# Performance work log

Measured on AMD Instinct MI355X. Metric: run time of the kernel, lower is better.

## Reference

```python
import jax, jax.numpy as jnp
import numpy as np

IN_NF, IN_EF, OUT_NF, H1, H2, H_IN = 16, 8, 16, 8, 8, 16
N_NODES, N_EDGES = 100000, 2000000


def _mlp(x, w1, b1, w2, b2):
    # Linear -> LeakyReLU(0.2) -> Linear
    return jax.nn.leaky_relu(x @ w1 + b1, negative_slope=0.2) @ w2 + b2


def setup_inputs() -> dict:
    key = jax.random.key(0)
    ks = jax.random.split(key, 20)
    d_in = 2 * IN_NF + IN_EF  # 40
    inp = {
        "nf": jax.random.normal(ks[0], (N_NODES, IN_NF), jnp.float32),
        "src_out": jax.random.randint(ks[1], (N_EDGES,), 0, N_NODES),
        "dst_out": jax.random.randint(ks[2], (N_EDGES,), 0, N_NODES),
        "nef_out": jax.random.normal(ks[3], (N_EDGES, IN_EF), jnp.float32),
        "src_in": jax.random.randint(ks[4], (N_EDGES,), 0, N_NODES),
        "dst_in": jax.random.randint(ks[5], (N_EDGES,), 0, N_NODES),
        "nef_in": jax.random.normal(ks[6], (N_EDGES, IN_EF), jnp.float32),
        # MLP_msg_o2i: (2*in_nf+in_ef) -> h_in -> out_nf
        "w_o2i1": jax.random.normal(ks[7], (d_in, H_IN), jnp.float32) * 0.1,
        "b_o2i1": jnp.zeros((H_IN,), jnp.float32),
        "w_o2i2": jax.random.normal(ks[8], (H_IN, OUT_NF), jnp.float32) * 0.1,
        "b_o2i2": jnp.zeros((OUT_NF,), jnp.float32),
        # MLP_msg_i2o: (2*in_nf+in_ef) -> h_in -> 1+h1+h2
        "w_i2o1": jax.random.normal(ks[9], (d_in, H_IN), jnp.float32) * 0.1,
        "b_i2o1": jnp.zeros((H_IN,), jnp.float32),
        "w_i2o2": jax.random.normal(ks[10], (H_IN, 1 + H1 + H2), jnp.float32) * 0.1,
        "b_i2o2": jnp.zeros((1 + H1 + H2,), jnp.float32),
        # MLP_reduce_o: (in_nf+h1+h2) -> h_in -> out_nf  (note: in_nf==out_nf here)
        "w_red1": jax.random.normal(ks[11], (OUT_NF + H1 + H2, H_IN), jnp.float32) * 0.1,
        "b_red1": jnp.zeros((H_IN,), jnp.float32),
        "w_red2": jax.random.normal(ks[12], (H_IN, OUT_NF), jnp.float32) * 0.1,
        "b_red2": jnp.zeros((OUT_NF,), jnp.float32),
    }
    return inp


def reference(nf, src_out, dst_out, nef_out, src_in, dst_in, nef_in,
              w_o2i1, b_o2i1, w_o2i2, b_o2i2,
              w_i2o1, b_i2o1, w_i2o2, b_i2o2,
              w_red1, b_red1, w_red2, b_red2):
    n = nf.shape[0]
    # --- update_all over 'net_out': edge gather-concat -> MLP -> scatter sum
    x_o = jnp.concatenate([nf[src_out], nf[dst_out], nef_out], axis=1)  # [E, 40]
    efi = _mlp(x_o, w_o2i1, b_o2i1, w_o2i2, b_o2i2)                      # [E, out_nf]
    new_nf = jax.ops.segment_sum(efi, dst_out, num_segments=n)           # overwrites 'new_nf'
    # --- apply_edges over 'net_in': gated messages
    x_i = jnp.concatenate([nf[src_in], nf[dst_in], nef_in], axis=1)      # [E, 40]
    m = _mlp(x_i, w_i2o1, b_i2o1, w_i2o2, b_i2o2)                        # [E, 1+h1+h2]
    k = jax.nn.sigmoid(m[:, :1])
    efo1 = m[:, 1:1 + H1] * k
    efo2 = m[:, 1 + H1:] * k
    # --- scatter sum / mean into dst nodes
    nfo1 = jax.ops.segment_sum(efo1, dst_in, num_segments=n)
    cnt = jax.ops.segment_sum(jnp.ones((dst_in.shape[0],), nf.dtype), dst_in, num_segments=n)
    nfo2 = jax.ops.segment_sum(efo2, dst_in, num_segments=n) / jnp.maximum(cnt, 1.0)[:, None]
    # --- apply_nodes only on net_in destination nodes; others keep new_nf
    reduced = _mlp(jnp.concatenate([new_nf, nfo1, nfo2], axis=1), w_red1, b_red1, w_red2, b_red2)
    has_in = (cnt > 0)[:, None]
    return jnp.where(has_in, reduced, new_nf)
```

## Files before the change

kernel.cpp:

```cpp
#include <hip/hip_runtime.h>
#include <math.h>

#define IN_NF 16
#define IN_EF 8
#define OUT_NF 16
#define H1 8
#define H2 8
#define H_IN 16
#define D_IN 40
#define NT 4
#define SCAN_NB 128

__device__ __forceinline__ unsigned int f2bf_bits(float f) {
    unsigned int u = __float_as_uint(f);
    u += 0x7FFFu + ((u >> 16) & 1u);
    return u >> 16;
}
__device__ __forceinline__ float bf_lo(unsigned int w) { return __uint_as_float(w << 16); }
__device__ __forceinline__ float bf_hi(unsigned int w) { return __uint_as_float(w & 0xFFFF0000u); }

__device__ __forceinline__ void unpack16(const unsigned short* base, float* x) {
    const uint4* p = (const uint4*)base;
    uint4 a = p[0], b = p[1];
    x[0]=bf_lo(a.x);  x[1]=bf_hi(a.x);  x[2]=bf_lo(a.y);  x[3]=bf_hi(a.y);
    x[4]=bf_lo(a.z);  x[5]=bf_hi(a.z);  x[6]=bf_lo(a.w);  x[7]=bf_hi(a.w);
    x[8]=bf_lo(b.x);  x[9]=bf_hi(b.x);  x[10]=bf_lo(b.y); x[11]=bf_hi(b.y);
    x[12]=bf_lo(b.z); x[13]=bf_hi(b.z); x[14]=bf_lo(b.w); x[15]=bf_hi(b.w);
}

__global__ __launch_bounds__(256) void k_tobf16(
    const float* __restrict__ nf, unsigned short* __restrict__ nf16, int n_nodes)
{
    int n = blockIdx.x * blockDim.x + threadIdx.x;
    if (n >= n_nodes) return;
    const float4* p = (const float4*)(nf + (long)n * IN_NF);
    unsigned int w[8];
#pragma unroll
    for (int q = 0; q < 4; ++q) {
        float4 v = p[q];
        w[2*q+0] = f2bf_bits(v.x) | (f2bf_bits(v.y) << 16);
        w[2*q+1] = f2bf_bits(v.z) | (f2bf_bits(v.w) << 16);
    }
    uint4* o = (uint4*)(nf16 + (size_t)n * 16);
    o[0] = make_uint4(w[0], w[1], w[2], w[3]);
    o[1] = make_uint4(w[4], w[5], w[6], w[7]);
}

__global__ __launch_bounds__(256) void k_hist(
    const int* __restrict__ dst_out, const int* __restrict__ dst_in,
    int* __restrict__ off_out, int* __restrict__ off_in, int n_edges)
{
    int i = (blockIdx.x * blockDim.x + threadIdx.x) * 4;
    if (i + 3 < n_edges) {
        int4 a = *(const int4*)(dst_out + i);
        atomicAdd(&off_out[a.x], 1); atomicAdd(&off_out[a.y], 1);
        atomicAdd(&off_out[a.z], 1); atomicAdd(&off_out[a.w], 1);
        int4 b = *(const int4*)(dst_in + i);
        atomicAdd(&off_in[b.x], 1); atomicAdd(&off_in[b.y], 1);
        atomicAdd(&off_in[b.z], 1); atomicAdd(&off_in[b.w], 1);
    } else {
        for (int e = i; e < n_edges; ++e) {
            atomicAdd(&off_out[dst_out[e]], 1);
            atomicAdd(&off_in[dst_in[e]], 1);
        }
    }
}

__global__ __launch_bounds__(256) void k_scan_partial(
    const int* __restrict__ a0, const int* __restrict__ a1, int n,
    int* __restrict__ bsum)
{
    int arr = blockIdx.x >> 7;
    int blk = blockIdx.x & (SCAN_NB - 1);
    const int* a = arr ? a1 : a0;
    int chunk = (n + SCAN_NB - 1) / SCAN_NB;
    int beg = blk * chunk;
    int end = min(beg + chunk, n);
    int s = 0;
    for (int i = beg + threadIdx.x; i < end; i += 256) s += a[i];
    __shared__ int sm[256];
    int t = threadIdx.x;
    sm[t] = s;
    __syncthreads();
    for (int d = 128; d > 0; d >>= 1) {
        if (t < d) sm[t] += sm[t + d];
        __syncthreads();
    }
    if (t == 0) bsum[arr * SCAN_NB + blk] = sm[0];
}

__global__ __launch_bounds__(64) void k_scan_bsum(int* __restrict__ bsum)
{
    int arr = threadIdx.x;
    if (arr >= 2) return;
    int run = 0;
    for (int i = 0; i < SCAN_NB; ++i) {
        int v = bsum[arr * SCAN_NB + i];
        bsum[arr * SCAN_NB + i] = run;
        run += v;
    }
}

__global__ __launch_bounds__(256) void k_scan_final(
    int* __restrict__ a0, int* __restrict__ a1, int n,
    const int* __restrict__ bsum)
{
    int arr = blockIdx.x >> 7;
    int blk = blockIdx.x & (SCAN_NB - 1);
    int* a = arr ? a1 : a0;
    int chunk = (n + SCAN_NB - 1) / SCAN_NB;
    int beg = blk * chunk;
    int end = min(beg + chunk, n);
    int t = threadIdx.x;
    __shared__ int sm[256];
    __shared__ int carry_sm;
    if (t == 0) carry_sm = bsum[arr * SCAN_NB + blk];
    __syncthreads();
    for (int base = beg; base < end; base += 256) {
        int i = base + t;
        int v = (i < end) ? a[i] : 0;
        sm[t] = v;
        __syncthreads();
        for (int d = 1; d < 256; d <<= 1) {
            int u = (t >= d) ? sm[t - d] : 0;
            __syncthreads();
            sm[t] += u;
            __syncthreads();
        }
        int carry = carry_sm;
        if (i < end) a[i] = carry + sm[t] - v;
        __syncthreads();
        if (t == 0) carry_sm = carry + sm[255];
        __syncthreads();
    }
}

__global__ __launch_bounds__(256, 4) void k_edge_a(
    const unsigned short* __restrict__ nf16,
    const int* __restrict__ src, const int* __restrict__ dst,
    const float* __restrict__ nef,
    const float* __restrict__ W1, const float* __restrict__ B1,
    const float* __restrict__ W2, const float* __restrict__ B2,
    int* __restrict__ cursor, unsigned short* __restrict__ msg, int n_edges)
{
    int e = blockIdx.x * blockDim.x + threadIdx.x;
    if (e >= n_edges) return;
    int s = src[e];
    int d = dst[e];

    float xs[IN_NF], xd[IN_NF], xe[IN_EF];
    unpack16(nf16 + (size_t)s * 16, xs);
    unpack16(nf16 + (size_t)d * 16, xd);
    {
        const float4* pe = (const float4*)(nef + (long)e * IN_EF);
#pragma unroll
        for (int q = 0; q < 2; ++q) {
            float4 v = pe[q];
            xe[4*q+0]=v.x; xe[4*q+1]=v.y; xe[4*q+2]=v.z; xe[4*q+3]=v.w;
        }
    }

    float h[H_IN];
#pragma unroll
    for (int j = 0; j < H_IN; ++j) h[j] = B1[j];
#pragma unroll
    for (int k = 0; k < IN_NF; ++k) {
        float a0 = xs[k], a1 = xd[k];
#pragma unroll
        for (int j = 0; j < H_IN; ++j) {
            h[j] = fmaf(a0, W1[k * H_IN + j], h[j]);
            h[j] = fmaf(a1, W1[(IN_NF + k) * H_IN + j], h[j]);
        }
    }
#pragma unroll
    for (int k = 0; k < IN_EF; ++k) {
        float a0 = xe[k];
#pragma unroll
        for (int j = 0; j < H_IN; ++j)
            h[j] = fmaf(a0, W1[(2 * IN_NF + k) * H_IN + j], h[j]);
    }
#pragma unroll
    for (int j = 0; j < H_IN; ++j) h[j] = (h[j] >= 0.f) ? h[j] : 0.2f * h[j];

    float o[OUT_NF];
#pragma unroll
    for (int j = 0; j < OUT_NF; ++j) o[j] = B2[j];
#pragma unroll
    for (int k = 0; k < H_IN; ++k) {
        float hk = h[k];
#pragma unroll
        for (int j = 0; j < OUT_NF; ++j) o[j] = fmaf(hk, W2[k * OUT_NF + j], o[j]);
    }

    int p = atomicAdd(&cursor[d], 1);
    unsigned int w[8];
#pragma unroll
    for (int q = 0; q < 8; ++q)
        w[q] = f2bf_bits(o[2 * q]) | (f2bf_bits(o[2 * q + 1]) << 16);
    uint4* pm = (uint4*)(msg + (size_t)p * 16);
    pm[0] = make_uint4(w[0], w[1], w[2], w[3]);
    pm[1] = make_uint4(w[4], w[5], w[6], w[7]);
}

__global__ __launch_bounds__(256, 4) void k_edge_b(
    const unsigned short* __restrict__ nf16,
    const int* __restrict__ src, const int* __restrict__ dst,
    const float* __restrict__ nef,
    const float* __restrict__ W1, const float* __restrict__ B1,
    const float* __restrict__ W2, const float* __restrict__ B2,
    int* __restrict__ cursor, unsigned short* __restrict__ msg, int n_edges)
{
    int e = blockIdx.x * blockDim.x + threadIdx.x;
    if (e >= n_edges) return;
    int s = src[e];
    int d = dst[e];

    float xs[IN_NF], xd[IN_NF], xe[IN_EF];
    unpack16(nf16 + (size_t)s * 16, xs);
    unpack16(nf16 + (size_t)d * 16, xd);
    {
        const float4* pe = (const float4*)(nef + (long)e * IN_EF);
#pragma unroll
        for (int q = 0; q < 2; ++q) {
            float4 v = pe[q];
            xe[4*q+0]=v.x; xe[4*q+1]=v.y; xe[4*q+2]=v.z; xe[4*q+3]=v.w;
        }
    }

    float h[H_IN];
#pragma unroll
    for (int j = 0; j < H_IN; ++j) h[j] = B1[j];
#pragma unroll
    for (int k = 0; k < IN_NF; ++k) {
        float a0 = xs[k], a1 = xd[k];
#pragma unroll
        for (int j = 0; j < H_IN; ++j) {
            h[j] = fmaf(a0, W1[k * H_IN + j], h[j]);
            h[j] = fmaf(a1, W1[(IN_NF + k) * H_IN + j], h[j]);
        }
    }
#pragma unroll
    for (int k = 0; k < IN_EF; ++k) {
        float a0 = xe[k];
#pragma unroll
        for (int j = 0; j < H_IN; ++j)
            h[j] = fmaf(a0, W1[(2 * IN_NF + k) * H_IN + j], h[j]);
    }
#pragma unroll
    for (int j = 0; j < H_IN; ++j) h[j] = (h[j] >= 0.f) ? h[j] : 0.2f * h[j];

    const int M = 1 + H1 + H2;
    float o[17];
#pragma unroll
    for (int j = 0; j < M; ++j) o[j] = B2[j];
#pragma unroll
    for (int k = 0; k < H_IN; ++k) {
        float hk = h[k];
#pragma unroll
        for (int j = 0; j < M; ++j) o[j] = fmaf(hk, W2[k * M + j], o[j]);
    }
    float g = 1.f / (1.f + __expf(-o[0]));

    int p = atomicAdd(&cursor[d], 1);
    unsigned int w[8];
#pragma unroll
    for (int q = 0; q < 8; ++q)
        w[q] = f2bf_bits(o[1 + 2*q] * g) | (f2bf_bits(o[2 + 2*q] * g) << 16);
    uint4* pm = (uint4*)(msg + (size_t)p * 16);
    pm[0] = make_uint4(w[0], w[1], w[2], w[3]);
    pm[1] = make_uint4(w[4], w[5], w[6], w[7]);
}

__global__ __launch_bounds__(256, 4) void k_gather(
    const int* __restrict__ curA, const int* __restrict__ curB,
    const unsigned short* __restrict__ msgA, const unsigned short* __restrict__ msgB,
    const float* __restrict__ w_red1, const float* __restrict__ b_red1,
    const float* __restrict__ w_red2, const float* __restrict__ b_red2,
    float* __restrict__ out, int n_nodes)
{
    int tid = blockIdx.x * blockDim.x + threadIdx.x;
    int node = tid >> 2;
    int t = tid & (NT - 1);
    if (node >= n_nodes) return;

    int begA = (node == 0) ? 0 : curA[node - 1];
    int endA = curA[node];
    int begB = (node == 0) ? 0 : curB[node - 1];
    int endB = curB[node];

    float accA[16], accB[16];
#pragma unroll
    for (int j = 0; j < 16; ++j) { accA[j] = 0.f; accB[j] = 0.f; }

    for (int i = begA + t; i < endA; i += NT) {
        const uint4* p = (const uint4*)(msgA + (size_t)i * 16);
        uint4 v0 = p[0], v1 = p[1];
        unsigned int w0=v0.x,w1=v0.y,w2=v0.z,w3=v0.w,w4=v1.x,w5=v1.y,w6=v1.z,w7=v1.w;
        accA[0]+=bf_lo(w0); accA[1]+=bf_hi(w0); accA[2]+=bf_lo(w1); accA[3]+=bf_hi(w1);
        accA[4]+=bf_lo(w2); accA[5]+=bf_hi(w2); accA[6]+=bf_lo(w3); accA[7]+=bf_hi(w3);
        accA[8]+=bf_lo(w4); accA[9]+=bf_hi(w4); accA[10]+=bf_lo(w5); accA[11]+=bf_hi(w5);
        accA[12]+=bf_lo(w6); accA[13]+=bf_hi(w6); accA[14]+=bf_lo(w7); accA[15]+=bf_hi(w7);
    }
    for (int i = begB + t; i < endB; i += NT) {
        const uint4* p = (const uint4*)(msgB + (size_t)i * 16);
        uint4 v0 = p[0], v1 = p[1];
        unsigned int w0=v0.x,w1=v0.y,w2=v0.z,w3=v0.w,w4=v1.x,w5=v1.y,w6=v1.z,w7=v1.w;
        accB[0]+=bf_lo(w0); accB[1]+=bf_hi(w0); accB[2]+=bf_lo(w1); accB[3]+=bf_hi(w1);
        accB[4]+=bf_lo(w2); accB[5]+=bf_hi(w2); accB[6]+=bf_lo(w3); accB[7]+=bf_hi(w3);
        accB[8]+=bf_lo(w4); accB[9]+=bf_hi(w4); accB[10]+=bf_lo(w5); accB[11]+=bf_hi(w5);
        accB[12]+=bf_lo(w6); accB[13]+=bf_hi(w6); accB[14]+=bf_lo(w7); accB[15]+=bf_hi(w7);
    }

#pragma unroll
    for (int mask = 1; mask < NT; mask <<= 1) {
#pragma unroll
        for (int j = 0; j < 16; ++j) {
            accA[j] += __shfl_xor(accA[j], mask);
            accB[j] += __shfl_xor(accB[j], mask);
        }
    }
    if (t != 0) return;

    int deg = endB - begB;
// ... 240 lines not shown

    float o[OUT_NF];
#pragma unroll
    for (int j = 0; j < OUT_NF; ++j) o[j] = b_red2[j];
#pragma unroll
    for (int k = 0; k < H_IN; ++k) {
        float hk = h[k];
#pragma unroll
        for (int j = 0; j < OUT_NF; ++j) o[j] = fmaf(hk, w_red2[k * OUT_NF + j], o[j]);
    }

    bool has_in = (deg > 0);
    float4* po = (float4*)(out + (long)node * OUT_NF);
#pragma unroll
    for (int i = 0; i < 4; ++i) {
        float4 v;
        if (has_in) { v.x=o[4*i+0]; v.y=o[4*i+1]; v.z=o[4*i+2]; v.w=o[4*i+3]; }
        else        { v.x=accA[4*i+0]; v.y=accA[4*i+1]; v.z=accA[4*i+2]; v.w=accA[4*i+3]; }
        po[i] = v;
    }
}

extern "C" void kernel_launch(void* const* d_in, const int* in_sizes, int n_in,
                              void* d_out, int out_size, void* d_ws, size_t ws_size,
                              hipStream_t stream) {
    const float* nf      = (const float*)d_in[0];
    const int*   src_out = (const int*)d_in[1];
    const int*   dst_out = (const int*)d_in[2];
    const float* nef_out = (const float*)d_in[3];
    const int*   src_in  = (const int*)d_in[4];
    const int*   dst_in  = (const int*)d_in[5];
    const float* nef_in  = (const float*)d_in[6];
    const float* w_o2i1  = (const float*)d_in[7];
    const float* b_o2i1  = (const float*)d_in[8];
    const float* w_o2i2  = (const float*)d_in[9];
    const float* b_o2i2  = (const float*)d_in[10];
    const float* w_i2o1  = (const float*)d_in[11];
    const float* b_i2o1  = (const float*)d_in[12];
    const float* w_i2o2  = (const float*)d_in[13];
    const float* b_i2o2  = (const float*)d_in[14];
    const float* w_red1  = (const float*)d_in[15];
    const float* b_red1  = (const float*)d_in[16];
    const float* w_red2  = (const float*)d_in[17];
    const float* b_red2  = (const float*)d_in[18];

    int n_nodes = in_sizes[0] / IN_NF;
    int n_edges = in_sizes[1];
    float* out = (float*)d_out;

    dim3 blk(256);
    dim3 egrid((n_edges + 255) / 256);
    dim3 hgrid((n_edges / 4 + 256) / 256 + 1);
    dim3 ngrid(((size_t)n_nodes * NT + 255) / 256);
    dim3 cgrid((n_nodes + 255) / 256);
    dim3 sgrid(2 * SCAN_NB);

    size_t off_bytes = (size_t)2 * n_nodes * sizeof(int);
    size_t nf16_bytes = (size_t)n_nodes * 16 * sizeof(unsigned short);
    size_t msg_bytes = (size_t)n_edges * 16 * sizeof(unsigned short);
    size_t need_fast = off_bytes + nf16_bytes + 2 * msg_bytes + 256;

    if (ws_size >= need_fast) {
        int* curA = (int*)d_ws;
        int* curB = curA + n_nodes;
        unsigned short* nf16 = (unsigned short*)(curB + n_nodes);
        unsigned short* msgA = nf16 + (size_t)n_nodes * 16;
        unsigned short* msgB = msgA + (size_t)n_edges * 16;
        int* bsum = (int*)msgA;

        hipMemsetAsync(d_ws, 0, off_bytes, stream);
        k_tobf16<<<cgrid, blk, 0, stream>>>(nf, nf16, n_nodes);
        k_hist<<<hgrid, blk, 0, stream>>>(dst_out, dst_in, curA, curB, n_edges);
        k_scan_partial<<<sgrid, blk, 0, stream>>>(curA, curB, n_nodes, bsum);
        k_scan_bsum<<<dim3(1), dim3(64), 0, stream>>>(bsum);
        k_scan_final<<<sgrid, blk, 0, stream>>>(curA, curB, n_nodes, bsum);
        k_edge_a<<<egrid, blk, 0, stream>>>(nf16, src_out, dst_out, nef_out,
                                            w_o2i1, b_o2i1, w_o2i2, b_o2i2,
                                            curA, msgA, n_edges);
        k_edge_b<<<egrid, blk, 0, stream>>>(nf16, src_in, dst_in, nef_in,
                                            w_i2o1, b_i2o1, w_i2o2, b_i2o2,
                                            curB, msgB, n_edges);
        k_gather<<<ngrid, blk, 0, stream>>>(curA, curB, msgA, msgB,
                                            w_red1, b_red1, w_red2, b_red2,
                                            out, n_nodes);
    } else {
        int* off_out  = (int*)d_ws;
        int* off_in   = off_out + n_nodes;
        int* perm_out = off_in + n_nodes;
        int* perm_in  = perm_out + n_edges;
        int* bsum = perm_out;

        hipMemsetAsync(d_ws, 0, off_bytes, stream);
        k_hist<<<hgrid, blk, 0, stream>>>(dst_out, dst_in, off_out, off_in, n_edges);
        k_scan_partial<<<sgrid, blk, 0, stream>>>(off_out, off_in, n_nodes, bsum);
        k_scan_bsum<<<dim3(1), dim3(64), 0, stream>>>(bsum);
        k_scan_final<<<sgrid, blk, 0, stream>>>(off_out, off_in, n_nodes, bsum);
        k_scatter<<<egrid, blk, 0, stream>>>(dst_out, dst_in, off_out, off_in,
                                             perm_out, perm_in, n_edges);
        k_node_fused<<<ngrid, blk, 0, stream>>>(nf, src_out, nef_out, src_in, nef_in,
                                          off_out, off_in, perm_out, perm_in,
                                          w_o2i1, b_o2i1, w_o2i2, b_o2i2,
                                          w_i2o1, b_i2o1, w_i2o2, b_i2o2,
                                          w_red1, b_red1, w_red2, b_red2,
                                          out, n_nodes);
    }
}
```

Measured before the change: 524.4 us.

## Use persistent grid-stride edge kernels with two edges per thread and prefetch

The edge MLP kernels become persistent, launched with a fixed grid of 1280 blocks. Each thread handles two edges per iteration and prefetches the next src/dst indices while computing, so gather latency overlaps with the FMA work and the cursor atomics. The bf16 conversion and the histogram kernels are merged into one launch to save a kernel launch. The extra live state may raise register pressure under the launch_bounds occupancy of 4.

```diff
diff --git a/kernel.cpp b/kernel.cpp
--- a/kernel.cpp
+++ b/kernel.cpp
@@ -10,6 +10,7 @@
 #define D_IN 40
 #define NT 4
 #define SCAN_NB 128
+#define EDGE_BLOCKS 1280
 
 __device__ __forceinline__ unsigned int f2bf_bits(float f) {
     unsigned int u = __float_as_uint(f);
@@ -19,31 +20,41 @@
 __device__ __forceinline__ float bf_lo(unsigned int w) { return __uint_as_float(w << 16); }
 __device__ __forceinline__ float bf_hi(unsigned int w) { return __uint_as_float(w & 0xFFFF0000u); }
 
-__device__ __forceinline__ void unpack16(const unsigned short* base, float* x) {
-    const uint4* p = (const uint4*)base;
-    uint4 a = p[0], b = p[1];
-    x[0]=bf_lo(a.x);  x[1]=bf_hi(a.x);  x[2]=bf_lo(a.y);  x[3]=bf_hi(a.y);
-    x[4]=bf_lo(a.z);  x[5]=bf_hi(a.z);  x[6]=bf_lo(a.w);  x[7]=bf_hi(a.w);
-    x[8]=bf_lo(b.x);  x[9]=bf_hi(b.x);  x[10]=bf_lo(b.y); x[11]=bf_hi(b.y);
-    x[12]=bf_lo(b.z); x[13]=bf_hi(b.z); x[14]=bf_lo(b.w); x[15]=bf_hi(b.w);
-}
-
-__global__ __launch_bounds__(256) void k_tobf16(
-    const float* __restrict__ nf, unsigned short* __restrict__ nf16, int n_nodes)
-{
-    int n = blockIdx.x * blockDim.x + threadIdx.x;
-    if (n >= n_nodes) return;
-    const float4* p = (const float4*)(nf + (long)n * IN_NF);
-    unsigned int w[8];
-#pragma unroll
-    for (int q = 0; q < 4; ++q) {
-        float4 v = p[q];
-        w[2*q+0] = f2bf_bits(v.x) | (f2bf_bits(v.y) << 16);
-        w[2*q+1] = f2bf_bits(v.z) | (f2bf_bits(v.w) << 16);
-    }
-    uint4* o = (uint4*)(nf16 + (size_t)n * 16);
-    o[0] = make_uint4(w[0], w[1], w[2], w[3]);
-    o[1] = make_uint4(w[4], w[5], w[6], w[7]);
+__global__ __launch_bounds__(256) void k_pre(
+    const float* __restrict__ nf, unsigned short* __restrict__ nf16, int n_nodes,
+    const int* __restrict__ dst_out, const int* __restrict__ dst_in,
+    int* __restrict__ curA, int* __restrict__ curB, int n_edges, int nb_conv)
+{
+    if ((int)blockIdx.x < nb_conv) {
+        int n = blockIdx.x * 256 + threadIdx.x;
+        if (n >= n_nodes) return;
+        const float4* p = (const float4*)(nf + (long)n * IN_NF);
+        unsigned int w[8];
+#pragma unroll
+        for (int q = 0; q < 4; ++q) {
+            float4 v = p[q];
+            w[2*q+0] = f2bf_bits(v.x) | (f2bf_bits(v.y) << 16);
+            w[2*q+1] = f2bf_bits(v.z) | (f2bf_bits(v.w) << 16);
+        }
+        uint4* o = (uint4*)(nf16 + (size_t)n * 16);
+        o[0] = make_uint4(w[0], w[1], w[2], w[3]);
+        o[1] = make_uint4(w[4], w[5], w[6], w[7]);
+    } else {
+        int i = ((blockIdx.x - nb_conv) * 256 + threadIdx.x) * 4;
+        if (i + 3 < n_edges) {
+            int4 a = *(const int4*)(dst_out + i);
+            atomicAdd(&curA[a.x], 1); atomicAdd(&curA[a.y], 1);
+            atomicAdd(&curA[a.z], 1); atomicAdd(&curA[a.w], 1);
+            int4 b = *(const int4*)(dst_in + i);
+            atomicAdd(&curB[b.x], 1); atomicAdd(&curB[b.y], 1);
+            atomicAdd(&curB[b.z], 1); atomicAdd(&curB[b.w], 1);
+        } else {
+            for (int e = i; e < n_edges; ++e) {
+                atomicAdd(&curA[dst_out[e]], 1);
+                atomicAdd(&curB[dst_in[e]], 1);
+            }
+        }
+    }
 }
 
 __global__ __launch_bounds__(256) void k_hist(
@@ -141,65 +152,151 @@
     const float* __restrict__ nef,
     const float* __restrict__ W1, const float* __restrict__ B1,
     const float* __restrict__ W2, const float* __restrict__ B2,
-    int* __restrict__ cursor, unsigned short* __restrict__ msg, int n_edges)
-{
-    int e = blockIdx.x * blockDim.x + threadIdx.x;
-    if (e >= n_edges) return;
-    int s = src[e];
-    int d = dst[e];
-
-    float xs[IN_NF], xd[IN_NF], xe[IN_EF];
-    unpack16(nf16 + (size_t)s * 16, xs);
-    unpack16(nf16 + (size_t)d * 16, xd);
-    {
-        const float4* pe = (const float4*)(nef + (long)e * IN_EF);
-#pragma unroll
-        for (int q = 0; q < 2; ++q) {
-            float4 v = pe[q];
-            xe[4*q+0]=v.x; xe[4*q+1]=v.y; xe[4*q+2]=v.z; xe[4*q+3]=v.w;
-        }
-    }
-
-    float h[H_IN];
-#pragma unroll
-    for (int j = 0; j < H_IN; ++j) h[j] = B1[j];
-#pragma unroll
-    for (int k = 0; k < IN_NF; ++k) {
-        float a0 = xs[k], a1 = xd[k];
-#pragma unroll
-        for (int j = 0; j < H_IN; ++j) {
-            h[j] = fmaf(a0, W1[k * H_IN + j], h[j]);
-            h[j] = fmaf(a1, W1[(IN_NF + k) * H_IN + j], h[j]);
-        }
-    }
-#pragma unroll
-    for (int k = 0; k < IN_EF; ++k) {
-        float a0 = xe[k];
-#pragma unroll
-        for (int j = 0; j < H_IN; ++j)
-            h[j] = fmaf(a0, W1[(2 * IN_NF + k) * H_IN + j], h[j]);
-    }
-#pragma unroll
-    for (int j = 0; j < H_IN; ++j) h[j] = (h[j] >= 0.f) ? h[j] : 0.2f * h[j];
-
-    float o[OUT_NF];
-#pragma unroll
-    for (int j = 0; j < OUT_NF; ++j) o[j] = B2[j];
-#pragma unroll
-    for (int k = 0; k < H_IN; ++k) {
-        float hk = h[k];
-#pragma unroll
-        for (int j = 0; j < OUT_NF; ++j) o[j] = fmaf(hk, W2[k * OUT_NF + j], o[j]);
-    }
-
-    int p = atomicAdd(&cursor[d], 1);
-    unsigned int w[8];
-#pragma unroll
-    for (int q = 0; q < 8; ++q)
-        w[q] = f2bf_bits(o[2 * q]) | (f2bf_bits(o[2 * q + 1]) << 16);
-    uint4* pm = (uint4*)(msg + (size_t)p * 16);
-    pm[0] = make_uint4(w[0], w[1], w[2], w[3]);
-    pm[1] = make_uint4(w[4], w[5], w[6], w[7]);
+    int* __restrict__ cursor, unsigned short* __restrict__ msg,
+    int n_edges, int T)
+{
+    int tid = blockIdx.x * blockDim.x + threadIdx.x;
+    int T2 = T * 2;
+
+    int e0 = tid, e1 = tid + T;
+    bool p0 = e0 < n_edges;
+    bool p1 = e1 < n_edges;
+    int s0 = 0, d0 = 0, s1 = 0, d1 = 0;
+    if (p0) { s0 = src[e0]; d0 = dst[e0]; }
+    if (p1) { s1 = src[e1]; d1 = dst[e1]; }
+
+    while (p0) {
+        const uint4* pS0 = (const uint4*)(nf16 + (size_t)s0 * 16);
+        uint4 Sa = pS0[0], Sb = pS0[1];
+        const uint4* pD0 = (const uint4*)(nf16 + (size_t)d0 * 16);
+        uint4 Da = pD0[0], Db = pD0[1];
+        const float4* pN0 = (const float4*)(nef + (size_t)e0 * IN_EF);
+        float4 Na = pN0[0], Nb = pN0[1];
+        uint4 Sc, Sd, Dc, Dd; float4 Nc, Nd;
+        if (p1) {
+            const uint4* pS1 = (const uint4*)(nf16 + (size_t)s1 * 16);
+            Sc = pS1[0]; Sd = pS1[1];
+            const uint4* pD1 = (const uint4*)(nf16 + (size_t)d1 * 16);
+            Dc = pD1[0]; Dd = pD1[1];
+            const float4* pN1 = (const float4*)(nef + (size_t)e1 * IN_EF);
+            Nc = pN1[0]; Nd = pN1[1];
+        }
+        int slot0 = atomicAdd(&cursor[d0], 1);
+        int slot1 = p1 ? atomicAdd(&cursor[d1], 1) : 0;
+        int f0 = e0 + T2, f1 = e1 + T2;
+        bool q0 = f0 < n_edges, q1 = f1 < n_edges;
+        int ts0 = 0, td0 = 0, ts1 = 0, td1 = 0;
+        if (q0) { ts0 = src[f0]; td0 = dst[f0]; }
+        if (q1) { ts1 = src[f1]; td1 = dst[f1]; }
+
+        {
+            float h[H_IN];
+#pragma unroll
+            for (int j = 0; j < H_IN; ++j) h[j] = B1[j];
+            unsigned int wS[8] = {Sa.x,Sa.y,Sa.z,Sa.w,Sb.x,Sb.y,Sb.z,Sb.w};
+            unsigned int wD[8] = {Da.x,Da.y,Da.z,Da.w,Db.x,Db.y,Db.z,Db.w};
+#pragma unroll
+            for (int w = 0; w < 8; ++w) {
+                float a0 = bf_lo(wS[w]), a1 = bf_hi(wS[w]);
+                float b0 = bf_lo(wD[w]), b1 = bf_hi(wD[w]);
+                const float* r0 = W1 + (2*w) * H_IN;
+                const float* r1 = W1 + (2*w+1) * H_IN;
+                const float* r2 = W1 + (IN_NF + 2*w) * H_IN;
+                const float* r3 = W1 + (IN_NF + 2*w+1) * H_IN;
+#pragma unroll
+                for (int j = 0; j < H_IN; ++j) {
+                    h[j] = fmaf(a0, r0[j], h[j]);
+                    h[j] = fmaf(a1, r1[j], h[j]);
+                    h[j] = fmaf(b0, r2[j], h[j]);
+                    h[j] = fmaf(b1, r3[j], h[j]);
+                }
+            }
+            float nv[8] = {Na.x,Na.y,Na.z,Na.w,Nb.x,Nb.y,Nb.z,Nb.w};
+#pragma unroll
+            for (int k = 0; k < IN_EF; ++k) {
+                const float* r = W1 + (2*IN_NF + k) * H_IN;
+                float a0 = nv[k];
+#pragma unroll
+                for (int j = 0; j < H_IN; ++j) h[j] = fmaf(a0, r[j], h[j]);
+            }
+#pragma unroll
+            for (int j = 0; j < H_IN; ++j) h[j] = (h[j] >= 0.f) ? h[j] : 0.2f * h[j];
+
+            float o[OUT_NF];
+#pragma unroll
+            for (int j = 0; j < OUT_NF; ++j) o[j] = B2[j];
+#pragma unroll
+            for (int k = 0; k < H_IN; ++k) {
+                float hk = h[k];
+                const float* r = W2 + k * OUT_NF;
+#pragma unroll
+                for (int j = 0; j < OUT_NF; ++j) o[j] = fmaf(hk, r[j], o[j]);
+            }
+            unsigned int w[8];
+#pragma unroll
+            for (int q = 0; q < 8; ++q)
+                w[q] = f2bf_bits(o[2*q]) | (f2bf_bits(o[2*q+1]) << 16);
+            uint4* pm = (uint4*)(msg + (size_t)slot0 * 16);
+            pm[0] = make_uint4(w[0], w[1], w[2], w[3]);
+            pm[1] = make_uint4(w[4], w[5], w[6], w[7]);
+        }
+
+        if (p1) {
+            float h[H_IN];
+#pragma unroll
+            for (int j = 0; j < H_IN; ++j) h[j] = B1[j];
+            unsigned int wS[8] = {Sc.x,Sc.y,Sc.z,Sc.w,Sd.x,Sd.y,Sd.z,Sd.w};
+            unsigned int wD[8] = {Dc.x,Dc.y,Dc.z,Dc.w,Dd.x,Dd.y,Dd.z,Dd.w};
+#pragma unroll
+            for (int w = 0; w < 8; ++w) {
+                float a0 = bf_lo(wS[w]), a1 = bf_hi(wS[w]);
+                float b0 = bf_lo(wD[w]), b1 = bf_hi(wD[w]);
+                const float* r0 = W1 + (2*w) * H_IN;
+                const float* r1 = W1 + (2*w+1) * H_IN;
+                const float* r2 = W1 + (IN_NF + 2*w) * H_IN;
+                const float* r3 = W1 + (IN_NF + 2*w+1) * H_IN;
+#pragma unroll
+                for (int j = 0; j < H_IN; ++j) {
+                    h[j] = fmaf(a0, r0[j], h[j]);
+                    h[j] = fmaf(a1, r1[j], h[j]);
+                    h[j] = fmaf(b0, r2[j], h[j]);
+                    h[j] = fmaf(b1, r3[j], h[j]);
+                }
+            }
+            float nv[8] = {Nc.x,Nc.y,Nc.z,Nc.w,Nd.x,Nd.y,Nd.z,Nd.w};
+#pragma unroll
+            for (int k = 0; k < IN_EF; ++k) {
+                const float* r = W1 + (2*IN_NF + k) * H_IN;
+                float a0 = nv[k];
+#pragma unroll
+                for (int j = 0; j < H_IN; ++j) h[j] = fmaf(a0, r[j], h[j]);
+            }
+#pragma unroll
+            for (int j = 0; j < H_IN; ++j) h[j] = (h[j] >= 0.f) ? h[j] : 0.2f * h[j];
+
+            float o[OUT_NF];
+#pragma unroll
+            for (int j = 0; j < OUT_NF; ++j) o[j] = B2[j];
+#pragma unroll
+            for (int k = 0; k < H_IN; ++k) {
+                float hk = h[k];
+                const float* r = W2 + k * OUT_NF;
+#pragma unroll
+                for (int j = 0; j < OUT_NF; ++j) o[j] = fmaf(hk, r[j], o[j]);
+            }
+            unsigned int w[8];
+#pragma unroll
+            for (int q = 0; q < 8; ++q)
+                w[q] = f2bf_bits(o[2*q]) | (f2bf_bits(o[2*q+1]) << 16);
+            uint4* pm = (uint4*)(msg + (size_t)slot1 * 16);
+            pm[0] = make_uint4(w[0], w[1], w[2], w[3]);
+            pm[1] = make_uint4(w[4], w[5], w[6], w[7]);
+        }
+
+        e0 = f0; e1 = f1;
+        s0 = ts0; d0 = td0; s1 = ts1; d1 = td1;
+        p0 = q0; p1 = q1;
+    }
 }
 
 __global__ __launch_bounds__(256, 4) void k_edge_b(
@@ -208,67 +305,154 @@
     const float* __restrict__ nef,
     const float* __restrict__ W1, const float* __restrict__ B1,
     const float* __restrict__ W2, const float* __restrict__ B2,
-    int* __restrict__ cursor, unsigned short* __restrict__ msg, int n_edges)
-{
-    int e = blockIdx.x * blockDim.x + threadIdx.x;
-    if (e >= n_edges) return;
-    int s = src[e];
-    int d = dst[e];
-
-    float xs[IN_NF], xd[IN_NF], xe[IN_EF];
-    unpack16(nf16 + (size_t)s * 16, xs);
-    unpack16(nf16 + (size_t)d * 16, xd);
-    {
-        const float4* pe = (const float4*)(nef + (long)e * IN_EF);
-#pragma unroll
-        for (int q = 0; q < 2; ++q) {
-            float4 v = pe[q];
-            xe[4*q+0]=v.x; xe[4*q+1]=v.y; xe[4*q+2]=v.z; xe[4*q+3]=v.w;
-        }
-    }
-
-    float h[H_IN];
-#pragma unroll
-    for (int j = 0; j < H_IN; ++j) h[j] = B1[j];
-#pragma unroll
-    for (int k = 0; k < IN_NF; ++k) {
-        float a0 = xs[k], a1 = xd[k];
-#pragma unroll
-        for (int j = 0; j < H_IN; ++j) {
-            h[j] = fmaf(a0, W1[k * H_IN + j], h[j]);
-            h[j] = fmaf(a1, W1[(IN_NF + k) * H_IN + j], h[j]);
-        }
-    }
-#pragma unroll
-    for (int k = 0; k < IN_EF; ++k) {
-        float a0 = xe[k];
-#pragma unroll
-        for (int j = 0; j < H_IN; ++j)
-            h[j] = fmaf(a0, W1[(2 * IN_NF + k) * H_IN + j], h[j]);
-    }
-#pragma unroll
-    for (int j = 0; j < H_IN; ++j) h[j] = (h[j] >= 0.f) ? h[j] : 0.2f * h[j];
-
+    int* __restrict__ cursor, unsigned short* __restrict__ msg,
+    int n_edges, int T)
+{
+    int tid = blockIdx.x * blockDim.x + threadIdx.x;
+    int T2 = T * 2;
     const int M = 1 + H1 + H2;
-    float o[17];
-#pragma unroll
-    for (int j = 0; j < M; ++j) o[j] = B2[j];
-#pragma unroll
-    for (int k = 0; k < H_IN; ++k) {
-        float hk = h[k];
-#pragma unroll
-        for (int j = 0; j < M; ++j) o[j] = fmaf(hk, W2[k * M + j], o[j]);
-    }
-    float g = 1.f / (1.f + __expf(-o[0]));
-
-    int p = atomicAdd(&cursor[d], 1);
-    unsigned int w[8];
-#pragma unroll
-    for (int q = 0; q < 8; ++q)
-        w[q] = f2bf_bits(o[1 + 2*q] * g) | (f2bf_bits(o[2 + 2*q] * g) << 16);
-    uint4* pm = (uint4*)(msg + (size_t)p * 16);
-    pm[0] = make_uint4(w[0], w[1], w[2], w[3]);
-    pm[1] = make_uint4(w[4], w[5], w[6], w[7]);
+
+    int e0 = tid, e1 = tid + T;
+    bool p0 = e0 < n_edges;
+    bool p1 = e1 < n_edges;
+    int s0 = 0, d0 = 0, s1 = 0, d1 = 0;
+    if (p0) { s0 = src[e0]; d0 = dst[e0]; }
+    if (p1) { s1 = src[e1]; d1 = dst[e1]; }
+
+    while (p0) {
+        const uint4* pS0 = (const uint4*)(nf16 + (size_t)s0 * 16);
+        uint4 Sa = pS0[0], Sb = pS0[1];
+        const uint4* pD0 = (const uint4*)(nf16 + (size_t)d0 * 16);
+        uint4 Da = pD0[0], Db = pD0[1];
+        const float4* pN0 = (const float4*)(nef + (size_t)e0 * IN_EF);
+        float4 Na = pN0[0], Nb = pN0[1];
+        uint4 Sc, Sd, Dc, Dd; float4 Nc, Nd;
+        if (p1) {
+            const uint4* pS1 = (const uint4*)(nf16 + (size_t)s1 * 16);
+            Sc = pS1[0]; Sd = pS1[1];
+            const uint4* pD1 = (const uint4*)(nf16 + (size_t)d1 * 16);
+            Dc = pD1[0]; Dd = pD1[1];
+            const float4* pN1 = (const float4*)(nef + (size_t)e1 * IN_EF);
+            Nc = pN1[0]; Nd = pN1[1];
+        }
+        int slot0 = atomicAdd(&cursor[d0], 1);
+        int slot1 = p1 ? atomicAdd(&cursor[d1], 1) : 0;
+        int f0 = e0 + T2, f1 = e1 + T2;
+        bool q0 = f0 < n_edges, q1 = f1 < n_edges;
+        int ts0 = 0, td0 = 0, ts1 = 0, td1 = 0;
+        if (q0) { ts0 = src[f0]; td0 = dst[f0]; }
+        if (q1) { ts1 = src[f1]; td1 = dst[f1]; }
+
+        {
+            float h[H_IN];
+#pragma unroll
+            for (int j = 0; j < H_IN; ++j) h[j] = B1[j];
+            unsigned int wS[8] = {Sa.x,Sa.y,Sa.z,Sa.w,Sb.x,Sb.y,Sb.z,Sb.w};
+            unsigned int wD[8] = {Da.x,Da.y,Da.z,Da.w,Db.x,Db.y,Db.z,Db.w};
+#pragma unroll
+            for (int w = 0; w < 8; ++w) {
+                float a0 = bf_lo(wS[w]), a1 = bf_hi(wS[w]);
+                float b0 = bf_lo(wD[w]), b1 = bf_hi(wD[w]);
+                const float* r0 = W1 + (2*w) * H_IN;
+                const float* r1 = W1 + (2*w+1) * H_IN;
+                const float* r2 = W1 + (IN_NF + 2*w) * H_IN;
+                const float* r3 = W1 + (IN_NF + 2*w+1) * H_IN;
+#pragma unroll
+                for (int j = 0; j < H_IN; ++j) {
+                    h[j] = fmaf(a0, r0[j], h[j]);
+                    h[j] = fmaf(a1, r1[j], h[j]);
+                    h[j] = fmaf(b0, r2[j], h[j]);
+                    h[j] = fmaf(b1, r3[j], h[j]);
+                }
+            }
+            float nv[8] = {Na.x,Na.y,Na.z,Na.w,Nb.x,Nb.y,Nb.z,Nb.w};
+#pragma unroll
+            for (int k = 0; k < IN_EF; ++k) {
+                const float* r = W1 + (2*IN_NF + k) * H_IN;
+                float a0 = nv[k];
+#pragma unroll
+                for (int j = 0; j < H_IN; ++j) h[j] = fmaf(a0, r[j], h[j]);
+            }
+#pragma unroll
+            for (int j = 0; j < H_IN; ++j) h[j] = (h[j] >= 0.f) ? h[j] : 0.2f * h[j];
+
+            float o[17];
+#pragma unroll
+            for (int j = 0; j < M; ++j) o[j] = B2[j];
+#pragma unroll
+            for (int k = 0; k < H_IN; ++k) {
+                float hk = h[k];
+                const float* r = W2 + k * M;
+#pragma unroll
+                for (int j = 0; j < M; ++j) o[j] = fmaf(hk, r[j], o[j]);
+            }
+            float g = 1.f / (1.f + __expf(-o[0]));
+            unsigned int w[8];
+#pragma unroll
+            for (int q = 0; q < 8; ++q)
+                w[q] = f2bf_bits(o[1+2*q] * g) | (f2bf_bits(o[2+2*q] * g) << 16);
+            uint4* pm = (uint4*)(msg + (size_t)slot0 * 16);
+            pm[0] = make_uint4(w[0], w[1], w[2], w[3]);
+            pm[1] = make_uint4(w[4], w[5], w[6], w[7]);
+        }
+
+        if (p1) {
+            float h[H_IN];
+#pragma unroll
+            for (int j = 0; j < H_IN; ++j) h[j] = B1[j];
+            unsigned int wS[8] = {Sc.x,Sc.y,Sc.z,Sc.w,Sd.x,Sd.y,Sd.z,Sd.w};
+            unsigned int wD[8] = {Dc.x,Dc.y,Dc.z,Dc.w,Dd.x,Dd.y,Dd.z,Dd.w};
+#pragma unroll
+            for (int w = 0; w < 8; ++w) {
+                float a0 = bf_lo(wS[w]), a1 = bf_hi(wS[w]);
+                float b0 = bf_lo(wD[w]), b1 = bf_hi(wD[w]);
+                const float* r0 = W1 + (2*w) * H_IN;
+                const float* r1 = W1 + (2*w+1) * H_IN;
+                const float* r2 = W1 + (IN_NF + 2*w) * H_IN;
+                const float* r3 = W1 + (IN_NF + 2*w+1) * H_IN;
+#pragma unroll
+                for (int j = 0; j < H_IN; ++j) {
+                    h[j] = fmaf(a0, r0[j], h[j]);
+                    h[j] = fmaf(a1, r1[j], h[j]);
+                    h[j] = fmaf(b0, r2[j], h[j]);
+                    h[j] = fmaf(b1, r3[j], h[j]);
+                }
+            }
+            float nv[8] = {Nc.x,Nc.y,Nc.z,Nc.w,Nd.x,Nd.y,Nd.z,Nd.w};
+#pragma unroll
+            for (int k = 0; k < IN_EF; ++k) {
+                const float* r = W1 + (2*IN_NF + k) * H_IN;
+                float a0 = nv[k];
+#pragma unroll
+                for (int j = 0; j < H_IN; ++j) h[j] = fmaf(a0, r[j], h[j]);
+            }
+#pragma unroll
+            for (int j = 0; j < H_IN; ++j) h[j] = (h[j] >= 0.f) ? h[j] : 0.2f * h[j];
+
+            float o[17];
+#pragma unroll
+            for (int j = 0; j < M; ++j) o[j] = B2[j];
+#pragma unroll
+            for (int k = 0; k < H_IN; ++k) {
+                float hk = h[k];
+                const float* r = W2 + k * M;
+#pragma unroll
+                for (int j = 0; j < M; ++j) o[j] = fmaf(hk, r[j], o[j]);
+            }
+            float g = 1.f / (1.f + __expf(-o[0]));
+            unsigned int w[8];
+#pragma unroll
+            for (int q = 0; q < 8; ++q)
+                w[q] = f2bf_bits(o[1+2*q] * g) | (f2bf_bits(o[2+2*q] * g) << 16);
+            uint4* pm = (uint4*)(msg + (size_t)slot1 * 16);
+            pm[0] = make_uint4(w[0], w[1], w[2], w[3]);
+            pm[1] = make_uint4(w[4], w[5], w[6], w[7]);
+        }
+
+        e0 = f0; e1 = f1;
+        s0 = ts0; d0 = td0; s1 = ts1; d1 = td1;
+        p0 = q0; p1 = q1;
+    }
 }
 
 __global__ __launch_bounds__(256, 4) void k_gather(
@@ -615,7 +799,6 @@
     dim3 egrid((n_edges + 255) / 256);
     dim3 hgrid((n_edges / 4 + 256) / 256 + 1);
     dim3 ngrid(((size_t)n_nodes * NT + 255) / 256);
-    dim3 cgrid((n_nodes + 255) / 256);
     dim3 sgrid(2 * SCAN_NB);
 
     size_t off_bytes = (size_t)2 * n_nodes * sizeof(int);
@@ -631,18 +814,25 @@
         unsigned short* msgB = msgA + (size_t)n_edges * 16;
         int* bsum = (int*)msgA;
 
+        int nb_conv = (n_nodes + 255) / 256;
+        int nb_hist = (n_edges / 4 + 256) / 256 + 1;
+        dim3 pgrid(nb_conv + nb_hist);
+
+        int T = EDGE_BLOCKS * 256;
+        dim3 edge_grid(EDGE_BLOCKS);
+
         hipMemsetAsync(d_ws, 0, off_bytes, stream);
-        k_tobf16<<<cgrid, blk, 0, stream>>>(nf, nf16, n_nodes);
-        k_hist<<<hgrid, blk, 0, stream>>>(dst_out, dst_in, curA, curB, n_edges);
+        k_pre<<<pgrid, blk, 0, stream>>>(nf, nf16, n_nodes, dst_out, dst_in,
+                                         curA, curB, n_edges, nb_conv);
         k_scan_partial<<<sgrid, blk, 0, stream>>>(curA, curB, n_nodes, bsum);
         k_scan_bsum<<<dim3(1), dim3(64), 0, stream>>>(bsum);
         k_scan_final<<<sgrid, blk, 0, stream>>>(curA, curB, n_nodes, bsum);
-        k_edge_a<<<egrid, blk, 0, stream>>>(nf16, src_out, dst_out, nef_out,
-                                            w_o2i1, b_o2i1, w_o2i2, b_o2i2,
-                                            curA, msgA, n_edges);
-        k_edge_b<<<egrid, blk, 0, stream>>>(nf16, src_in, dst_in, nef_in,
-                                            w_i2o1, b_i2o1, w_i2o2, b_i2o2,
-                                            curB, msgB, n_edges);
+        k_edge_a<<<edge_grid, blk, 0, stream>>>(nf16, src_out, dst_out, nef_out,
+                                                w_o2i1, b_o2i1, w_o2i2, b_o2i2,
+                                                curA, msgA, n_edges, T);
+        k_edge_b<<<edge_grid, blk, 0, stream>>>(nf16, src_in, dst_in, nef_in,
+                                                w_i2o1, b_i2o1, w_i2o2, b_i2o2,
+                                                curB, msgB, n_edges, T);
         k_gather<<<ngrid, blk, 0, stream>>>(curA, curB, msgA, msgB,
                                             w_red1, b_red1, w_red2, b_red2,
                                             out, n_nodes);
```

Result: slower. 747.9 us (+42.6%).

## Merge edge MLP kernels and pre-pass kernels into single launches

Applied to the files above, without the earlier changes.

Fuses the bf16 conversion and histogram kernels into one launch split by block index, and merges the two edge-MLP kernels into one launch where the first half of blocks handles net_out and the second half net_in. Also issues the cursor atomic early, ahead of the MLP math, to overlap its latency, and writes messages with nontemporal stores. This cuts launch count and tail gaps and lets the two edge phases overlap, but block-uniform branching on weight pointers may defeat scalar constant loads and raise register pressure.

```diff
diff --git a/kernel.cpp b/kernel.cpp
--- a/kernel.cpp
+++ b/kernel.cpp
@@ -11,6 +11,8 @@
 #define NT 4
 #define SCAN_NB 128
 
+typedef unsigned int uivec4 __attribute__((ext_vector_type(4)));
+
 __device__ __forceinline__ unsigned int f2bf_bits(float f) {
     unsigned int u = __float_as_uint(f);
     u += 0x7FFFu + ((u >> 16) & 1u);
@@ -19,31 +21,41 @@
 __device__ __forceinline__ float bf_lo(unsigned int w) { return __uint_as_float(w << 16); }
 __device__ __forceinline__ float bf_hi(unsigned int w) { return __uint_as_float(w & 0xFFFF0000u); }
 
-__device__ __forceinline__ void unpack16(const unsigned short* base, float* x) {
-    const uint4* p = (const uint4*)base;
-    uint4 a = p[0], b = p[1];
-    x[0]=bf_lo(a.x);  x[1]=bf_hi(a.x);  x[2]=bf_lo(a.y);  x[3]=bf_hi(a.y);
-    x[4]=bf_lo(a.z);  x[5]=bf_hi(a.z);  x[6]=bf_lo(a.w);  x[7]=bf_hi(a.w);
-    x[8]=bf_lo(b.x);  x[9]=bf_hi(b.x);  x[10]=bf_lo(b.y); x[11]=bf_hi(b.y);
-    x[12]=bf_lo(b.z); x[13]=bf_hi(b.z); x[14]=bf_lo(b.w); x[15]=bf_hi(b.w);
-}
-
-__global__ __launch_bounds__(256) void k_tobf16(
-    const float* __restrict__ nf, unsigned short* __restrict__ nf16, int n_nodes)
-{
-    int n = blockIdx.x * blockDim.x + threadIdx.x;
-    if (n >= n_nodes) return;
-    const float4* p = (const float4*)(nf + (long)n * IN_NF);
-    unsigned int w[8];
-#pragma unroll
-    for (int q = 0; q < 4; ++q) {
-        float4 v = p[q];
-        w[2*q+0] = f2bf_bits(v.x) | (f2bf_bits(v.y) << 16);
-        w[2*q+1] = f2bf_bits(v.z) | (f2bf_bits(v.w) << 16);
-    }
-    uint4* o = (uint4*)(nf16 + (size_t)n * 16);
-    o[0] = make_uint4(w[0], w[1], w[2], w[3]);
-    o[1] = make_uint4(w[4], w[5], w[6], w[7]);
+__global__ __launch_bounds__(256) void k_pre(
+    const float* __restrict__ nf, unsigned short* __restrict__ nf16, int n_nodes,
+    const int* __restrict__ dst_out, const int* __restrict__ dst_in,
+    int* __restrict__ curA, int* __restrict__ curB, int n_edges, int nb_conv)
+{
+    if ((int)blockIdx.x < nb_conv) {
+        int n = blockIdx.x * 256 + threadIdx.x;
+        if (n >= n_nodes) return;
+        const float4* p = (const float4*)(nf + (long)n * IN_NF);
+        unsigned int w[8];
+#pragma unroll
+        for (int q = 0; q < 4; ++q) {
+            float4 v = p[q];
+            w[2*q+0] = f2bf_bits(v.x) | (f2bf_bits(v.y) << 16);
+            w[2*q+1] = f2bf_bits(v.z) | (f2bf_bits(v.w) << 16);
+        }
+        uint4* o = (uint4*)(nf16 + (size_t)n * 16);
+        o[0] = make_uint4(w[0], w[1], w[2], w[3]);
+        o[1] = make_uint4(w[4], w[5], w[6], w[7]);
+    } else {
+        int i = ((blockIdx.x - nb_conv) * 256 + threadIdx.x) * 4;
+        if (i + 3 < n_edges) {
+            int4 a = *(const int4*)(dst_out + i);
+            atomicAdd(&curA[a.x], 1); atomicAdd(&curA[a.y], 1);
+            atomicAdd(&curA[a.z], 1); atomicAdd(&curA[a.w], 1);
+            int4 b = *(const int4*)(dst_in + i);
+            atomicAdd(&curB[b.x], 1); atomicAdd(&curB[b.y], 1);
+            atomicAdd(&curB[b.z], 1); atomicAdd(&curB[b.w], 1);
+        } else {
+            for (int e = i; e < n_edges; ++e) {
+                atomicAdd(&curA[dst_out[e]], 1);
+                atomicAdd(&curB[dst_in[e]], 1);
+            }
+        }
+    }
 }
 
 __global__ __launch_bounds__(256) void k_hist(
@@ -135,140 +147,117 @@
     }
 }
 
-__global__ __launch_bounds__(256, 4) void k_edge_a(
+__global__ __launch_bounds__(256, 4) void k_edges(
     const unsigned short* __restrict__ nf16,
-    const int* __restrict__ src, const int* __restrict__ dst,
-    const float* __restrict__ nef,
-    const float* __restrict__ W1, const float* __restrict__ B1,
-    const float* __restrict__ W2, const float* __restrict__ B2,
-    int* __restrict__ cursor, unsigned short* __restrict__ msg, int n_edges)
-{
-    int e = blockIdx.x * blockDim.x + threadIdx.x;
+    const int* __restrict__ srcA, const int* __restrict__ dstA,
+    const float* __restrict__ nefA,
+    const int* __restrict__ srcB, const int* __restrict__ dstB,
+    const float* __restrict__ nefB,
+    const float* __restrict__ W1A, const float* __restrict__ B1A,
+    const float* __restrict__ W2A, const float* __restrict__ B2A,
+    const float* __restrict__ W1B, const float* __restrict__ B1B,
+    const float* __restrict__ W2B, const float* __restrict__ B2B,
+    int* __restrict__ curA, int* __restrict__ curB,
+    unsigned short* __restrict__ msgA, unsigned short* __restrict__ msgB,
+    int n_edges, int nbe)
+{
+    bool isA = (int)blockIdx.x < nbe;
+    int bid = isA ? (int)blockIdx.x : (int)blockIdx.x - nbe;
+    int e = bid * 256 + (int)threadIdx.x;
     if (e >= n_edges) return;
+
+    const int* src = isA ? srcA : srcB;
+    const int* dst = isA ? dstA : dstB;
+    const float* nef = isA ? nefA : nefB;
+    const float* W1 = isA ? W1A : W1B;
+    const float* B1 = isA ? B1A : B1B;
+    int* cursor = isA ? curA : curB;
+    unsigned short* msg = isA ? msgA : msgB;
+
     int s = src[e];
     int d = dst[e];
 
-    float xs[IN_NF], xd[IN_NF], xe[IN_EF];
-    unpack16(nf16 + (size_t)s * 16, xs);
-    unpack16(nf16 + (size_t)d * 16, xd);
+    const uint4* pS = (const uint4*)(nf16 + (size_t)s * 16);
+    uint4 Sa = pS[0], Sb = pS[1];
+    const uint4* pD = (const uint4*)(nf16 + (size_t)d * 16);
+    uint4 Da = pD[0], Db = pD[1];
+    const float4* pN = (const float4*)(nef + (size_t)e * IN_EF);
+    float4 Na = pN[0], Nb = pN[1];
+
+    int slot = atomicAdd(&cursor[d], 1);
+
+    float h[H_IN];
+#pragma unroll
+    for (int j = 0; j < H_IN; ++j) h[j] = B1[j];
     {
-        const float4* pe = (const float4*)(nef + (long)e * IN_EF);
-#pragma unroll
-        for (int q = 0; q < 2; ++q) {
-            float4 v = pe[q];
-            xe[4*q+0]=v.x; xe[4*q+1]=v.y; xe[4*q+2]=v.z; xe[4*q+3]=v.w;
-        }
-    }
-
-    float h[H_IN];
-#pragma unroll
-    for (int j = 0; j < H_IN; ++j) h[j] = B1[j];
-#pragma unroll
-    for (int k = 0; k < IN_NF; ++k) {
-        float a0 = xs[k], a1 = xd[k];
-#pragma unroll
-        for (int j = 0; j < H_IN; ++j) {
-            h[j] = fmaf(a0, W1[k * H_IN + j], h[j]);
-            h[j] = fmaf(a1, W1[(IN_NF + k) * H_IN + j], h[j]);
-        }
-    }
-#pragma unroll
-    for (int k = 0; k < IN_EF; ++k) {
-        float a0 = xe[k];
-#pragma unroll
-        for (int j = 0; j < H_IN; ++j)
-            h[j] = fmaf(a0, W1[(2 * IN_NF + k) * H_IN + j], h[j]);
+        unsigned int wS[8] = {Sa.x,Sa.y,Sa.z,Sa.w,Sb.x,Sb.y,Sb.z,Sb.w};
+        unsigned int wD[8] = {Da.x,Da.y,Da.z,Da.w,Db.x,Db.y,Db.z,Db.w};
+#pragma unroll
+        for (int w = 0; w < 8; ++w) {
+            float a0 = bf_lo(wS[w]), a1 = bf_hi(wS[w]);
+            float b0 = bf_lo(wD[w]), b1 = bf_hi(wD[w]);
+            const float* r0 = W1 + (2*w) * H_IN;
+            const float* r1 = W1 + (2*w+1) * H_IN;
+            const float* r2 = W1 + (IN_NF + 2*w) * H_IN;
+            const float* r3 = W1 + (IN_NF + 2*w+1) * H_IN;
+#pragma unroll
+            for (int j = 0; j < H_IN; ++j) {
+                h[j] = fmaf(a0, r0[j], h[j]);
+                h[j] = fmaf(a1, r1[j], h[j]);
+                h[j] = fmaf(b0, r2[j], h[j]);
+                h[j] = fmaf(b1, r3[j], h[j]);
+            }
+        }
+        float nv[8] = {Na.x,Na.y,Na.z,Na.w,Nb.x,Nb.y,Nb.z,Nb.w};
+#pragma unroll
+        for (int k = 0; k < IN_EF; ++k) {
+            const float* r = W1 + (2*IN_NF + k) * H_IN;
+            float a0 = nv[k];
+#pragma unroll
+            for (int j = 0; j < H_IN; ++j) h[j] = fmaf(a0, r[j], h[j]);
+        }
     }
 #pragma unroll
     for (int j = 0; j < H_IN; ++j) h[j] = (h[j] >= 0.f) ? h[j] : 0.2f * h[j];
 
-    float o[OUT_NF];
-#pragma unroll
-    for (int j = 0; j < OUT_NF; ++j) o[j] = B2[j];
-#pragma unroll
-    for (int k = 0; k < H_IN; ++k) {
-        float hk = h[k];
-#pragma unroll
-        for (int j = 0; j < OUT_NF; ++j) o[j] = fmaf(hk, W2[k * OUT_NF + j], o[j]);
-    }
-
-    int p = atomicAdd(&cursor[d], 1);
     unsigned int w[8];
-#pragma unroll
-    for (int q = 0; q < 8; ++q)
-        w[q] = f2bf_bits(o[2 * q]) | (f2bf_bits(o[2 * q + 1]) << 16);
-    uint4* pm = (uint4*)(msg + (size_t)p * 16);
-    pm[0] = make_uint4(w[0], w[1], w[2], w[3]);
-    pm[1] = make_uint4(w[4], w[5], w[6], w[7]);
-}
-
-__global__ __launch_bounds__(256, 4) void k_edge_b(
-    const unsigned short* __restrict__ nf16,
-    const int* __restrict__ src, const int* __restrict__ dst,
-    const float* __restrict__ nef,
-    const float* __restrict__ W1, const float* __restrict__ B1,
-    const float* __restrict__ W2, const float* __restrict__ B2,
-    int* __restrict__ cursor, unsigned short* __restrict__ msg, int n_edges)
-{
-    int e = blockIdx.x * blockDim.x + threadIdx.x;
-    if (e >= n_edges) return;
-    int s = src[e];
-    int d = dst[e];
-
-    float xs[IN_NF], xd[IN_NF], xe[IN_EF];
-    unpack16(nf16 + (size_t)s * 16, xs);
-    unpack16(nf16 + (size_t)d * 16, xd);
-    {
-        const float4* pe = (const float4*)(nef + (long)e * IN_EF);
-#pragma unroll
-        for (int q = 0; q < 2; ++q) {
-            float4 v = pe[q];
-            xe[4*q+0]=v.x; xe[4*q+1]=v.y; xe[4*q+2]=v.z; xe[4*q+3]=v.w;
-        }
-    }
-
-    float h[H_IN];
-#pragma unroll
-    for (int j = 0; j < H_IN; ++j) h[j] = B1[j];
-#pragma unroll
-    for (int k = 0; k < IN_NF; ++k) {
-        float a0 = xs[k], a1 = xd[k];
-#pragma unroll
-        for (int j = 0; j < H_IN; ++j) {
-            h[j] = fmaf(a0, W1[k * H_IN + j], h[j]);
-            h[j] = fmaf(a1, W1[(IN_NF + k) * H_IN + j], h[j]);
-        }
-    }
-#pragma unroll
-    for (int k = 0; k < IN_EF; ++k) {
-        float a0 = xe[k];
-#pragma unroll
-        for (int j = 0; j < H_IN; ++j)
-            h[j] = fmaf(a0, W1[(2 * IN_NF + k) * H_IN + j], h[j]);
-    }
-#pragma unroll
-    for (int j = 0; j < H_IN; ++j) h[j] = (h[j] >= 0.f) ? h[j] : 0.2f * h[j];
-
-    const int M = 1 + H1 + H2;
-    float o[17];
-#pragma unroll
-    for (int j = 0; j < M; ++j) o[j] = B2[j];
-#pragma unroll
-    for (int k = 0; k < H_IN; ++k) {
-        float hk = h[k];
-#pragma unroll
-        for (int j = 0; j < M; ++j) o[j] = fmaf(hk, W2[k * M + j], o[j]);
-    }
-    float g = 1.f / (1.f + __expf(-o[0]));
-
-    int p = atomicAdd(&cursor[d], 1);
-    unsigned int w[8];
-#pragma unroll
-    for (int q = 0; q < 8; ++q)
-        w[q] = f2bf_bits(o[1 + 2*q] * g) | (f2bf_bits(o[2 + 2*q] * g) << 16);
-    uint4* pm = (uint4*)(msg + (size_t)p * 16);
-    pm[0] = make_uint4(w[0], w[1], w[2], w[3]);
-    pm[1] = make_uint4(w[4], w[5], w[6], w[7]);
+    if (isA) {
+        float o[OUT_NF];
+#pragma unroll
+        for (int j = 0; j < OUT_NF; ++j) o[j] = B2A[j];
+#pragma unroll
+        for (int k = 0; k < H_IN; ++k) {
+            float hk = h[k];
+            const float* r = W2A + k * OUT_NF;
+#pragma unroll
+            for (int j = 0; j < OUT_NF; ++j) o[j] = fmaf(hk, r[j], o[j]);
+        }
+#pragma unroll
+        for (int q = 0; q < 8; ++q)
+            w[q] = f2bf_bits(o[2*q]) | (f2bf_bits(o[2*q+1]) << 16);
+    } else {
+        const int M = 1 + H1 + H2;
+        float o[17];
+#pragma unroll
+        for (int j = 0; j < M; ++j) o[j] = B2B[j];
+#pragma unroll
+        for (int k = 0; k < H_IN; ++k) {
+            float hk = h[k];
+            const float* r = W2B + k * M;
+#pragma unroll
+            for (int j = 0; j < M; ++j) o[j] = fmaf(hk, r[j], o[j]);
+        }
+        float g = 1.f / (1.f + __expf(-o[0]));
+#pragma unroll
+        for (int q = 0; q < 8; ++q)
+            w[q] = f2bf_bits(o[1+2*q] * g) | (f2bf_bits(o[2+2*q] * g) << 16);
+    }
+
+    uivec4* pm = (uivec4*)(msg + (size_t)slot * 16);
+    uivec4 v0 = {w[0], w[1], w[2], w[3]};
+    uivec4 v1 = {w[4], w[5], w[6], w[7]};
+    __builtin_nontemporal_store(v0, pm);
+    __builtin_nontemporal_store(v1, pm + 1);
 }
 
 __global__ __launch_bounds__(256, 4) void k_gather(
@@ -615,7 +604,6 @@
     dim3 egrid((n_edges + 255) / 256);
     dim3 hgrid((n_edges / 4 + 256) / 256 + 1);
     dim3 ngrid(((size_t)n_nodes * NT + 255) / 256);
-    dim3 cgrid((n_nodes + 255) / 256);
     dim3 sgrid(2 * SCAN_NB);
 
     size_t off_bytes = (size_t)2 * n_nodes * sizeof(int);
@@ -631,18 +619,26 @@
         unsigned short* msgB = msgA + (size_t)n_edges * 16;
         int* bsum = (int*)msgA;
 
+        int nb_conv = (n_nodes + 255) / 256;
+        int nb_hist = (n_edges / 4 + 256) / 256 + 1;
+        dim3 pgrid(nb_conv + nb_hist);
+
+        int nbe = (n_edges + 255) / 256;
+        dim3 edge_grid(2 * nbe);
+
         hipMemsetAsync(d_ws, 0, off_bytes, stream);
-        k_tobf16<<<cgrid, blk, 0, stream>>>(nf, nf16, n_nodes);
-        k_hist<<<hgrid, blk, 0, stream>>>(dst_out, dst_in, curA, curB, n_edges);
+        k_pre<<<pgrid, blk, 0, stream>>>(nf, nf16, n_nodes, dst_out, dst_in,
+                                         curA, curB, n_edges, nb_conv);
         k_scan_partial<<<sgrid, blk, 0, stream>>>(curA, curB, n_nodes, bsum);
         k_scan_bsum<<<dim3(1), dim3(64), 0, stream>>>(bsum);
         k_scan_final<<<sgrid, blk, 0, stream>>>(curA, curB, n_nodes, bsum);
-        k_edge_a<<<egrid, blk, 0, stream>>>(nf16, src_out, dst_out, nef_out,
-                                            w_o2i1, b_o2i1, w_o2i2, b_o2i2,
-                                            curA, msgA, n_edges);
-        k_edge_b<<<egrid, blk, 0, stream>>>(nf16, src_in, dst_in, nef_in,
-                                            w_i2o1, b_i2o1, w_i2o2, b_i2o2,
-                                            curB, msgB, n_edges);
+        k_edges<<<edge_grid, blk, 0, stream>>>(nf16,
+                                               src_out, dst_out, nef_out,
+                                               src_in, dst_in, nef_in,
+                                               w_o2i1, b_o2i1, w_o2i2, b_o2i2,
+                                               w_i2o1, b_i2o1, w_i2o2, b_i2o2,
+                                               curA, curB, msgA, msgB,
+                                               n_edges, nbe);
         k_gather<<<ngrid, blk, 0, stream>>>(curA, curB, msgA, msgB,
                                             w_red1, b_red1, w_red2, b_red2,
                                             out, n_nodes);
```

After: 458.5 us. 12.6% less time.
